# Optimization experiments

Measured on AMD Instinct MI355X. Metric: run time of the kernel, lower is better.

The kernel has to match this reference:

```python
import jax, jax.numpy as jnp
import numpy as np

B, S, D, H, L, V = 8, 512, 1024, 16, 12, 30145
FF = 4 * D
NL = 2  # n_langs
EPS = 1e-12


def _ln(x, g, b):
    m = jnp.mean(x, axis=-1, keepdims=True)
    v = jnp.var(x, axis=-1, keepdims=True)
    return (x - m) * jax.lax.rsqrt(v + EPS) * g + b


def setup_inputs() -> dict:
    key = jax.random.key(0)
    ks = iter(jax.random.split(key, 32))
    std, estd = 0.02, 0.02
    d = {
        "input_ids": jax.random.randint(next(ks), (B, S), 0, V),
        "langs": jax.random.randint(next(ks), (B, S), 0, NL),
        "attention_mask": jnp.ones((B, S), jnp.float32),
        "word_emb": jax.random.normal(next(ks), (V, D), jnp.float32) * estd,
        "pos_emb": jax.random.normal(next(ks), (S, D), jnp.float32) * estd,
        "lang_emb": jax.random.normal(next(ks), (NL, D), jnp.float32) * estd,
        "ln_emb_g": jnp.ones((D,), jnp.float32),
        "ln_emb_b": jnp.zeros((D,), jnp.float32),
        "Wq": jax.random.normal(next(ks), (L, D, D), jnp.float32) * std,
        "bq": jnp.zeros((L, D), jnp.float32),
        "Wk": jax.random.normal(next(ks), (L, D, D), jnp.float32) * std,
        "bk": jnp.zeros((L, D), jnp.float32),
        "Wv": jax.random.normal(next(ks), (L, D, D), jnp.float32) * std,
        "bv": jnp.zeros((L, D), jnp.float32),
        "Wo": jax.random.normal(next(ks), (L, D, D), jnp.float32) * std,
        "bo": jnp.zeros((L, D), jnp.float32),
        "ln1_g": jnp.ones((L, D), jnp.float32),
        "ln1_b": jnp.zeros((L, D), jnp.float32),
        "W1": jax.random.normal(next(ks), (L, D, FF), jnp.float32) * std,
        "b1": jnp.zeros((L, FF), jnp.float32),
        "W2": jax.random.normal(next(ks), (L, FF, D), jnp.float32) * std,
        "b2": jnp.zeros((L, D), jnp.float32),
        "ln2_g": jnp.ones((L, D), jnp.float32),
        "ln2_b": jnp.zeros((L, D), jnp.float32),
    }
    return d


def reference(input_ids, langs, attention_mask, word_emb, pos_emb, lang_emb,
              ln_emb_g, ln_emb_b, Wq, bq, Wk, bk, Wv, bv, Wo, bo,
              ln1_g, ln1_b, W1, b1, W2, b2, ln2_g, ln2_b):
    dh = D // H
    scale = 1.0 / np.sqrt(dh).astype(np.float32)
    # embeddings: word + position + language, then LayerNorm, then pad-mask
    x = word_emb[input_ids] + pos_emb[None, :, :] + lang_emb[langs]  # [B,S,D]
    x = _ln(x, ln_emb_g, ln_emb_b)
    fmask = attention_mask  # [B,S], 1=keep
    x = x * fmask[:, :, None]
    neg = (-1e30) * (1.0 - fmask)[:, None, None, :]  # [B,1,1,S] additive mask

    def layer(x, p):
        Wq_, bq_, Wk_, bk_, Wv_, bv_, Wo_, bo_, g1, gb1, W1_, b1_, W2_, b2_, g2, gb2 = p
        q = ((x @ Wq_ + bq_) * scale).reshape(B, S, H, dh)
        k = (x @ Wk_ + bk_).reshape(B, S, H, dh)
        v = (x @ Wv_ + bv_).reshape(B, S, H, dh)
        scores = jnp.einsum('bqhd,bkhd->bhqk', q, k) + neg
        w = jax.nn.softmax(scores, axis=-1)
        ctx = jnp.einsum('bhqk,bkhd->bqhd', w, v).reshape(B, S, D)
        x = _ln(x + ctx @ Wo_ + bo_, g1, gb1)
        h = jax.nn.gelu(x @ W1_ + b1_, approximate=False)  # erf gelu as in source
        x = _ln(x + h @ W2_ + b2_, g2, gb2)
        x = x * fmask[:, :, None]
        return x, None

    params = (Wq, bq, Wk, bk, Wv, bv, Wo, bo, ln1_g, ln1_b, W1, b1, W2, b2, ln2_g, ln2_b)
    x, _ = jax.lax.scan(layer, x, params)
    return x
```

## Files before the change

### kernel.cpp

```cpp
#include <hip/hip_runtime.h>
#include <math.h>

typedef float  f32x4  __attribute__((ext_vector_type(4)));
typedef __bf16 bf16x8 __attribute__((ext_vector_type(8)));
typedef __bf16 bf16x4 __attribute__((ext_vector_type(4)));

#define DEV __device__ __forceinline__

DEV f32x4 mfma16(bf16x8 a, bf16x8 b, f32x4 c) {
    return __builtin_amdgcn_mfma_f32_16x16x32_bf16(a, b, c, 0, 0, 0);
}

DEV void async16(const void* g, void* l) {
    __builtin_amdgcn_global_load_lds((const __attribute__((address_space(1))) void*)g,
                                     (__attribute__((address_space(3))) void*)l, 16, 0, 0);
}

constexpr int B_  = 8;
constexpr int S_  = 512;
constexpr int D_  = 1024;
constexpr int H_  = 16;
constexpr int FF_ = 4096;
constexpr int ROWS = B_ * S_;

__global__ __launch_bounds__(256)
void embed_ln_kernel(const int* __restrict__ ids, const int* __restrict__ lgs,
                     const float* __restrict__ fmask,
                     const float* __restrict__ wemb, const float* __restrict__ pemb,
                     const float* __restrict__ lemb,
                     const float* __restrict__ g, const float* __restrict__ bb,
                     float* __restrict__ xf, __bf16* __restrict__ xb)
{
    __shared__ float2 red[4];
    const int row = blockIdx.x;
    const int s   = row & (S_ - 1);
    const int t   = threadIdx.x;
    const int lane = t & 63, w = t >> 6;
    const int id = ids[row], lg = lgs[row];

    float4 wv = *(const float4*)(wemb + ((size_t)id << 10) + t * 4);
    float4 pv = *(const float4*)(pemb + ((size_t)s  << 10) + t * 4);
    float4 lv = *(const float4*)(lemb + ((size_t)lg << 10) + t * 4);
    float a[4] = { wv.x + pv.x + lv.x, wv.y + pv.y + lv.y,
                   wv.z + pv.z + lv.z, wv.w + pv.w + lv.w };

    float sm = a[0] + a[1] + a[2] + a[3];
    float sq = a[0]*a[0] + a[1]*a[1] + a[2]*a[2] + a[3]*a[3];
#pragma unroll
    for (int o = 32; o > 0; o >>= 1) { sm += __shfl_down(sm, o); sq += __shfl_down(sq, o); }
    if (lane == 0) red[w] = make_float2(sm, sq);
    __syncthreads();
    float ts = red[0].x + red[1].x + red[2].x + red[3].x;
    float tq = red[0].y + red[1].y + red[2].y + red[3].y;
    float mean = ts * (1.0f / D_);
    float var  = tq * (1.0f / D_) - mean * mean;
    float rs   = rsqrtf(var + 1e-12f);
    float fm   = fmask[row];

    float4 gv = *(const float4*)(g  + t * 4);
    float4 bv = *(const float4*)(bb + t * 4);
    float o0 = ((a[0]-mean)*rs*gv.x + bv.x) * fm;
    float o1 = ((a[1]-mean)*rs*gv.y + bv.y) * fm;
    float o2 = ((a[2]-mean)*rs*gv.z + bv.z) * fm;
    float o3 = ((a[3]-mean)*rs*gv.w + bv.w) * fm;
    *(float4*)(xf + ((size_t)row << 10) + t * 4) = make_float4(o0, o1, o2, o3);
    bf16x4 ob; ob[0] = (__bf16)o0; ob[1] = (__bf16)o1; ob[2] = (__bf16)o2; ob[3] = (__bf16)o3;
    *(bf16x4*)(xb + ((size_t)row << 10) + t * 4) = ob;
}

template<int NP>
__global__ __launch_bounds__(256)
void ln_resN_kernel(const float* __restrict__ xin, const __bf16* __restrict__ yp,
                    const float* __restrict__ g, const float* __restrict__ bb,
                    const float* __restrict__ fmask,
                    float* __restrict__ xf_out, __bf16* __restrict__ xb_out)
{
    constexpr size_t MN = (size_t)ROWS * D_;
    __shared__ float2 red[4];
    const int row = blockIdx.x;
    const int t   = threadIdx.x;
    const int lane = t & 63, w = t >> 6;
    const size_t base = ((size_t)row << 10) + t * 4;

    float4 xv = *(const float4*)(xin + base);
    float a[4] = { xv.x, xv.y, xv.z, xv.w };
#pragma unroll
    for (int pslice = 0; pslice < NP; ++pslice) {
        bf16x4 yv = *(const bf16x4*)(yp + base + (size_t)pslice * MN);
#pragma unroll
        for (int j = 0; j < 4; ++j) a[j] += (float)yv[j];
    }

    float sm = a[0] + a[1] + a[2] + a[3];
    float sq = a[0]*a[0] + a[1]*a[1] + a[2]*a[2] + a[3]*a[3];
#pragma unroll
    for (int o = 32; o > 0; o >>= 1) { sm += __shfl_down(sm, o); sq += __shfl_down(sq, o); }
    if (lane == 0) red[w] = make_float2(sm, sq);
    __syncthreads();
    float ts = red[0].x + red[1].x + red[2].x + red[3].x;
    float tq = red[0].y + red[1].y + red[2].y + red[3].y;
    float mean = ts * (1.0f / D_);
    float var  = tq * (1.0f / D_) - mean * mean;
    float rs   = rsqrtf(var + 1e-12f);
    float fm   = fmask ? fmask[row] : 1.0f;

    float4 gv = *(const float4*)(g  + t * 4);
    float4 bv = *(const float4*)(bb + t * 4);
    float o0 = ((a[0]-mean)*rs*gv.x + bv.x) * fm;
    float o1 = ((a[1]-mean)*rs*gv.y + bv.y) * fm;
    float o2 = ((a[2]-mean)*rs*gv.z + bv.z) * fm;
    float o3 = ((a[3]-mean)*rs*gv.w + bv.w) * fm;
    *(float4*)(xf_out + base) = make_float4(o0, o1, o2, o3);
    bf16x4 ob; ob[0] = (__bf16)o0; ob[1] = (__bf16)o1; ob[2] = (__bf16)o2; ob[3] = (__bf16)o3;
    *(bf16x4*)(xb_out + base) = ob;
}

__global__ __launch_bounds__(256)
void conv_all_kernel(const float* __restrict__ Wq, const float* __restrict__ Wk,
                     const float* __restrict__ Wv, const float* __restrict__ Wo,
                     const float* __restrict__ W1, const float* __restrict__ W2,
                     __bf16* __restrict__ qkvT, __bf16* __restrict__ woT,
                     __bf16* __restrict__ w1T, __bf16* __restrict__ w2T)
{
    __shared__ __bf16 tile[64][66];
    const int id = blockIdx.x;
    const float* src; __bf16* dst; int K, N, t;
    if (id < 1024) {
        const int m = id >> 8; t = id & 255; K = 1024; N = 1024;
        src = (m == 0) ? Wq : (m == 1) ? Wk : (m == 2) ? Wv : Wo;
        dst = (m == 3) ? woT : qkvT + (size_t)m * 1024 * 1024;
    } else if (id < 2048) {
        t = id - 1024; K = 1024; N = 4096; src = W1; dst = w1T;
    } else {
        t = id - 2048; K = 4096; N = 1024; src = W2; dst = w2T;
    }
    const int ktiles = K >> 6;
    const int tk = t % ktiles, tn = t / ktiles;
    const int k0 = tk << 6, n0 = tn << 6;
    const int tt = threadIdx.x;
#pragma unroll
    for (int i = 0; i < 16; ++i) {
        int idx = i * 256 + tt;
        int r = idx >> 6, c = idx & 63;
        tile[c][r] = (__bf16)src[(size_t)(k0 + r) * N + n0 + c];
    }
    __syncthreads();
#pragma unroll
    for (int i = 0; i < 16; ++i) {
        int idx = i * 256 + tt;
        int r = idx >> 6, c = idx & 63;
        dst[(size_t)(n0 + r) * K + k0 + c] = tile[r][c];
    }
}

template<int EPI>
__global__ __launch_bounds__(512, 2)
void gemm256_kernel(const __bf16* __restrict__ A, const __bf16* __restrict__ Bt,
                    const float* __restrict__ b0, const float* __restrict__ b1,
                    const float* __restrict__ b2,
                    __bf16* __restrict__ o0, __bf16* __restrict__ o1,
                    __bf16* __restrict__ o2, __bf16* __restrict__ oP,
                    int M, int N, int K, int Kloc, int nTn, int tiles)
{
    __shared__ __bf16 lds[65536];
    const int tid  = threadIdx.x;
    const int lane = tid & 63;
    const int w    = tid >> 6;
    const int wr   = w >> 2, wc = w & 3;

    const int nwg = gridDim.x, bid = blockIdx.x;
    const int cpx = nwg >> 3;
    const int bswz = (bid & 7) * cpx + (bid >> 3);
    const int slice = bswz / tiles;
    const int tile  = bswz % tiles;
    const int bm = tile / nTn, bn = tile % nTn;
    const int m0 = bm << 8, n0 = bn << 8;
    const int ks = slice * Kloc;

    const int rrT = tid >> 3;
    const size_t swzK  = (size_t)(((tid & 7) ^ (rrT & 7)) * 8);
    const size_t aoff0 = (size_t)rrT * K + swzK;
    const size_t boff0 = (size_t)((rrT >> 5) * 64 + (rrT & 31)) * K + swzK;
    const size_t boff1 = (size_t)(((rrT >> 5) + 2) * 64 + (rrT & 31)) * K + swzK;
    const int wub = w * 512;

    const int aread = (wr * 64 + (lane & 15)) * 64;
    const int bread = (wc * 32 + (lane & 15)) * 64;
    const int csw0 = ((      (lane >> 4) * 16) ^ ((lane & 7) << 4)) >> 1;
    const int csw1 = ((64 +  (lane >> 4) * 16) ^ ((lane & 7) << 4)) >> 1;

    f32x4 acc[8][4] = {};
    bf16x8 a_[4][2], b_[2][2];

#define ST_A(p,h,kt) do {                                                     \
    const size_t gb = (size_t)(m0 + (h) * 64) * K + (kt);                     \
    async16(A + gb + aoff0,                  lds + ((p)*2+(h))*8192 + wub);   \
    async16(A + gb + (size_t)128*K + aoff0,  lds + ((p)*2+(h))*8192 + 4096 + wub); \
} while (0)
#define ST_B(p,h,kt) do {                                                     \
    const size_t gb = (size_t)(n0 + (h) * 32) * K + (kt);                     \
    async16(Bt + gb + boff0, lds + 32768 + ((p)*2+(h))*8192 + wub);           \
    async16(Bt + gb + boff1, lds + 32768 + ((p)*2+(h))*8192 + 4096 + wub);    \
} while (0)
#define DS_A(p,h) do {                                                        \
    const __bf16* base_ = lds + ((p)*2+(h))*8192 + aread;                     \
    _Pragma("unroll") for (int m_ = 0; m_ < 4; ++m_) {                        \
        a_[m_][0] = *(const bf16x8*)(base_ + m_*1024 + csw0);                 \
        a_[m_][1] = *(const bf16x8*)(base_ + m_*1024 + csw1);                 \
    }                                                                         \
} while (0)
#define DS_B(p,h) do {                                                        \
    const __bf16* base_ = lds + 32768 + ((p)*2+(h))*8192 + bread;             \
    _Pragma("unroll") for (int n_ = 0; n_ < 2; ++n_) {                        \
        b_[n_][0] = *(const bf16x8*)(base_ + n_*1024 + csw0);                 \
        b_[n_][1] = *(const bf16x8*)(base_ + n_*1024 + csw1);                 \
    }                                                                         \
} while (0)
#define MM(mb,nb) do {                                                        \
    _Pragma("unroll") for (int m_ = 0; m_ < 4; ++m_)                          \
    _Pragma("unroll") for (int n_ = 0; n_ < 2; ++n_)                          \
    _Pragma("unroll") for (int k_ = 0; k_ < 2; ++k_)                          \
        acc[(mb)+m_][(nb)+n_] = mfma16(a_[m_][k_], b_[n_][k_], acc[(mb)+m_][(nb)+n_]); \
} while (0)
#define SYNC do { __builtin_amdgcn_s_barrier();                               \
    asm volatile("s_waitcnt lgkmcnt(0)" ::: "memory");                        \
    __builtin_amdgcn_s_setprio(1); } while (0)
#define PEND do { __builtin_amdgcn_s_setprio(0);                              \
    __builtin_amdgcn_s_barrier(); } while (0)

    ST_A(0,0, ks);      ST_B(0,1, ks);      ST_A(0,1, ks);      ST_B(0,0, ks);
    ST_A(1,0, ks + 64); ST_B(1,1, ks + 64); ST_A(1,1, ks + 64);
    asm volatile("s_waitcnt vmcnt(6)" ::: "memory");
    __builtin_amdgcn_s_barrier();

    const int nIter = Kloc >> 7;
    for (int i = 0; i < nIter; ++i) {
        const bool nl = (i != nIter - 1);
        const int kt1 = ks + (2*i+1) * 64;
        const int kt2 = ks + (2*i+2) * 64;
        const int kt3 = kt2 + 64;
        DS_A(0,0); DS_B(0,0); ST_B(1,0,kt1);
        SYNC; MM(0,0); PEND;
        DS_B(0,1); if (nl) ST_A(0,0,kt2);
        SYNC; MM(0,2); PEND;
        DS_A(0,1); if (nl) ST_B(0,1,kt2);
        SYNC; MM(4,2); PEND;
        DS_B(0,0); if (nl) ST_A(0,1,kt2);
        SYNC; MM(4,0);
        __builtin_amdgcn_s_setprio(0);
        if (nl) asm volatile("s_waitcnt vmcnt(6)" ::: "memory");
        else    asm volatile("s_waitcnt vmcnt(0)" ::: "memory");
        __builtin_amdgcn_s_barrier();
        DS_A(1,0); DS_B(1,0); if (nl) ST_B(0,0,kt2);
        SYNC; MM(0,0); PEND;
        DS_B(1,1); if (nl) ST_A(1,0,kt3);
        SYNC; MM(0,2); PEND;
        DS_A(1,1); if (nl) ST_B(1,1,kt3);
        SYNC; MM(4,2); PEND;
        DS_B(1,0); if (nl) ST_A(1,1,kt3);
        SYNC; MM(4,0);
        __builtin_amdgcn_s_setprio(0);
        if (nl) asm volatile("s_waitcnt vmcnt(6)" ::: "memory");
        __builtin_amdgcn_s_barrier();
    }
#undef ST_A
#undef ST_B
#undef DS_A
#undef DS_B
#undef MM
#undef SYNC
#undef PEND

    const int mrow = m0 + wr * 128 + (lane >> 4) * 4;
    const int ncol = n0 + wc * 64 + (lane & 15);
    if (EPI == 0) {
        const int sel = n0 >> 10;
        const int nc = ncol & 1023;
        if (sel < 2) {
            __bf16* out = (sel == 0) ? o0 : o1;
            const float* bp = (sel == 0) ? b0 : b1;
            const float scl = (sel == 0) ? 0.125f : 1.0f;
#pragma unroll
            for (int ni = 0; ni < 4; ++ni) {
                const float bvv = bp[nc + ni * 16];
#pragma unroll
                for (int mi = 0; mi < 8; ++mi)
#pragma unroll
                    for (int r = 0; r < 4; ++r)
                        out[(size_t)(mrow + mi * 16 + r) * D_ + nc + ni * 16] =
                            (__bf16)((acc[mi][ni][r] + bvv) * scl);
            }
        } else {
#pragma unroll
            for (int ni = 0; ni < 4; ++ni) {
                const int dhf = nc + ni * 16;
                const float bvv = b2[dhf];
                const int hh = dhf >> 6, dh = dhf & 63;
#pragma unroll
                for (int mi = 0; mi < 8; ++mi) {
                    const int gm0 = mrow + mi * 16;
                    const int bb_ = gm0 >> 9, s0 = gm0 & 511;
                    bf16x4 pk;
#pragma unroll
                    for (int r = 0; r < 4; ++r) pk[r] = (__bf16)(acc[mi][ni][r] + bvv);
                    *(bf16x4*)(o2 + ((size_t)((bb_ * 16 + hh) * 64 + dh) << 9) + s0) = pk;
                }
            }
        }
    } else if (EPI == 2) {
#pragma unroll
        for (int ni = 0; ni < 4; ++ni) {
            const float bvv = b0[ncol + ni * 16];
#pragma unroll
            for (int mi = 0; mi < 8; ++mi)
#pragma unroll
                for (int r = 0; r < 4; ++r) {
                    float v = acc[mi][ni][r] + bvv;
                    float ge = 0.5f * v * (1.0f + erff(v * 0.70710678118654752f));
                    o0[(size_t)(mrow + mi * 16 + r) * N + ncol + ni * 16] = (__bf16)ge;
                }
        }
    } else {
        __bf16* Y = oP + (size_t)slice * M * N;
#pragma unroll
        for (int ni = 0; ni < 4; ++ni) {
            const float bvv = (slice == 0) ? b0[ncol + ni * 16] : 0.0f;
#pragma unroll
            for (int mi = 0; mi < 8; ++mi)
#pragma unroll
                for (int r = 0; r < 4; ++r)
                    Y[(size_t)(mrow + mi * 16 + r) * N + ncol + ni * 16] =
                        (__bf16)(acc[mi][ni][r] + bvv);
        }
    }
}

__global__ __launch_bounds__(256, 2)
void gemm_kernel(const __bf16* __restrict__ A, const __bf16* __restrict__ Bt,
                 const float* __restrict__ bias, __bf16* __restrict__ Cb,
                 int M, int N, int K)
{
    __shared__ __bf16 As[128 * 64];
    __shared__ __bf16 Bs[128 * 64];
    const int tid = threadIdx.x;
    const int lane = tid & 63;
    const int w = tid >> 6, wr = w >> 1, wc = w & 1;
    const int nT = N >> 7;
    const int nwg = gridDim.x;
    const int bid = blockIdx.x;
    const int cpx = nwg >> 3;
    const int bswz = (bid & 7) * cpx + (bid >> 3);
    const int bm = bswz / nT, bn = bswz % nT;
    const int m0 = bm << 7, n0 = bn << 7;

    f32x4 acc[4][4] = {};

    const int chr = tid >> 3, chc = tid & 7;
    const __bf16* ga = A  + (size_t)(m0 + chr) * K + chc * 8;
    const __bf16* gb = Bt + (size_t)(n0 + chr) * K + chc * 8;
    char* la = (char*)As + (tid & ~63) * 16;
    char* lb = (char*)Bs + (tid & ~63) * 16;

    const __bf16* arow = As + (wr * 64 + (lane & 15)) * 64 + (lane >> 4) * 8;
    const __bf16* brow = Bs + (wc * 64 + (lane & 15)) * 64 + (lane >> 4) * 8;

    for (int k0 = 0; k0 < K; k0 += 64) {
#pragma unroll
        for (int i = 0; i < 4; ++i) {
            async16(ga + (size_t)(i * 32) * K + k0, la + i * 4096);
            async16(gb + (size_t)(i * 32) * K + k0, lb + i * 4096);
        }
        __syncthreads();
#pragma unroll
        for (int kk = 0; kk < 2; ++kk) {
            bf16x8 af[4], bf[4];
#pragma unroll
            for (int i = 0; i < 4; ++i) af[i] = *(const bf16x8*)(arow + i * 16 * 64 + kk * 32);
#pragma unroll
            for (int i = 0; i < 4; ++i) bf[i] = *(const bf16x8*)(brow + i * 16 * 64 + kk * 32);
#pragma unroll
            for (int mi = 0; mi < 4; ++mi)
#pragma unroll
                for (int ni = 0; ni < 4; ++ni)
                    acc[mi][ni] = mfma16(af[mi], bf[ni], acc[mi][ni]);
        }
        __syncthreads();
    }

    const int mb = m0 + wr * 64 + ((lane >> 4) * 4);
    const int nb = n0 + wc * 64 + (lane & 15);
#pragma unroll
    for (int ni = 0; ni < 4; ++ni) {
        const float bvv = bias[nb + ni * 16];
#pragma unroll
        for (int mi = 0; mi < 4; ++mi)
#pragma unroll
            for (int r = 0; r < 4; ++r)
                Cb[(size_t)(mb + mi * 16 + r) * N + nb + ni * 16] =
                    (__bf16)(acc[mi][ni][r] + bvv);
    }
}

__global__ __launch_bounds__(256, 2)
void attn_kernel(const __bf16* __restrict__ q, const __bf16* __restrict__ k,
                 const __bf16* __restrict__ vT, const float* __restrict__ fmask,
                 __bf16* __restrict__ ctx)
{
    __shared__ __bf16 Ks[256 * 64];
    __shared__ __bf16 Vt[64 * 256];
    __shared__ float  negm[S_];
    const int bid = blockIdx.x;
    const int qt = bid & 7, h = (bid >> 3) & 15, b = bid >> 7;
    const int tid = threadIdx.x, lane = tid & 63, w = tid >> 6;
    const int g = lane >> 4, q15 = lane & 15, r7 = lane & 7;

    const __bf16* kbase  = k  + ((size_t)b * S_) * D_ + h * 64;
    const __bf16* vTbase = vT + ((size_t)((b * 16 + h) * 64) << 9);
    char* kl = (char*)Ks + (tid & ~63) * 16;
    char* vl = (char*)Vt + (tid & ~63) * 16;
    const int srow  = tid >> 3;
    const int sslot = (tid & 7) ^ (srow & 7);
    const int vrow  = tid >> 5;
#define ST_K(c) do { _Pragma("unroll") for (int i_ = 0; i_ < 8; ++i_) {       \
        const int s_ = (c) * 256 + i_ * 32 + srow;                            \
        async16(kbase + (size_t)s_ * D_ + sslot * 8, kl + i_ * 4096); } } while (0)
#define ST_V(c) do { _Pragma("unroll") for (int i_ = 0; i_ < 8; ++i_) {       \
        const int d_ = i_ * 8 + vrow;                                         \
        async16(vTbase + ((size_t)d_ << 9) + (c) * 256 +                      \
                (((tid & 31) ^ (d_ & 7)) << 3), vl + i_ * 4096); } } while (0)

    ST_K(0);
    for (int i = tid; i < S_; i += 256) negm[i] = (fmask[b * S_ + i] - 1.0f) * 1e30f;

    const __bf16* qbase = q + ((size_t)b * S_ + qt * 64 + w * 16) * D_ + h * 64;
    const bf16x8 qf0 = *(const bf16x8*)(qbase + (size_t)q15 * D_ + g * 8);
    const bf16x8 qf1 = *(const bf16x8*)(qbase + (size_t)q15 * D_ + 32 + g * 8);

    f32x4 sc[32];
#pragma unroll
    for (int i = 0; i < 32; ++i) { sc[i][0] = 0.f; sc[i][1] = 0.f; sc[i][2] = 0.f; sc[i][3] = 0.f; }

#define QKT(c) do { _Pragma("unroll") for (int nf = 0; nf < 16; ++nf) {       \
        const __bf16* kr = Ks + (nf * 16 + q15) * 64;                         \
        const bf16x8 kf0 = *(const bf16x8*)(kr + ((g ^ r7) << 3));            \
        const bf16x8 kf1 = *(const bf16x8*)(kr + (((g + 4) ^ r7) << 3));      \
        sc[(c)*16+nf] = mfma16(kf0, qf0, sc[(c)*16+nf]);                      \
        sc[(c)*16+nf] = mfma16(kf1, qf1, sc[(c)*16+nf]); } } while (0)

    __syncthreads();
    ST_V(0);
    QKT(0);
    __syncthreads();
    ST_K(1);
    __syncthreads();
    QKT(1);

    float mx = -3e38f;
#pragma unroll
    for (int i = 0; i < 32; ++i) {
        const float4 nm4 = *(const float4*)(negm + ((i >> 4) * 256 + (i & 15) * 16 + 4 * g));
        sc[i][0] += nm4.x; sc[i][1] += nm4.y; sc[i][2] += nm4.z; sc[i][3] += nm4.w;
        mx = fmaxf(mx, fmaxf(fmaxf(sc[i][0], sc[i][1]), fmaxf(sc[i][2], sc[i][3])));
    }
    mx = fmaxf(mx, __shfl_xor(mx, 16));
    mx = fmaxf(mx, __shfl_xor(mx, 32));
    float sum = 0.f;
#pragma unroll
    for (int i = 0; i < 32; ++i)
#pragma unroll
        for (int r = 0; r < 4; ++r) { float pp = __expf(sc[i][r] - mx); sc[i][r] = pp; sum += pp; }
    sum += __shfl_xor(sum, 16);
    sum += __shfl_xor(sum, 32);
    const float inv = 1.0f / sum;

    __bf16* P = Ks + w * 4096;
    f32x4 co[4] = {};
#define WR_P(c) do { _Pragma("unroll") for (int i_ = 0; i_ < 16; ++i_) {      \
        bf16x4 pk;                                                            \
        _Pragma("unroll") for (int r = 0; r < 4; ++r) pk[r] = (__bf16)sc[(c)*16+i_][r]; \
        *(bf16x4*)(P + q15 * 256 + ((i_ * 16 + 4 * g) ^ (8 * r7))) = pk; } } while (0)
#define PV() do { _Pragma("unroll") for (int kt = 0; kt < 8; ++kt) {          \
        const bf16x8 pf = *(const bf16x8*)(P + q15 * 256 + ((kt * 32 + 8 * g) ^ (8 * r7))); \
        _Pragma("unroll") for (int nf = 0; nf < 4; ++nf) {                    \
            const int d_ = nf * 16 + q15;                                     \
            const bf16x8 vf = *(const bf16x8*)(Vt + d_ * 256 + ((kt * 32 + 8 * g) ^ (8 * r7))); \
            co[nf] = mfma16(vf, pf, co[nf]); } } } while (0)

    __syncthreads();
    WR_P(0);
    __syncthreads();
    PV();
    __syncthreads();
    WR_P(1);
    ST_V(1);
    __syncthreads();
    PV();
#undef ST_K
#undef ST_V
#undef QKT
#undef WR_P
#undef PV

    __bf16* cb = ctx + ((size_t)b * S_ + qt * 64 + w * 16 + q15) * D_ + h * 64;
#pragma unroll
    for (int nf = 0; nf < 4; ++nf) {
        bf16x4 o4;
#pragma unroll
        for (int r = 0; r < 4; ++r) o4[r] = (__bf16)(co[nf][r] * inv);
        *(bf16x4*)(cb + nf * 16 + 4 * g) = o4;
    }
}

extern "C" void kernel_launch(void* const* d_in, const int* in_sizes, int n_in,
                              void* d_out, int out_size, void* d_ws, size_t ws_size,
                              hipStream_t stream)
{
    (void)in_sizes; (void)n_in; (void)out_size; (void)ws_size;
    const int*   ids   = (const int*)d_in[0];
    const int*   lgs   = (const int*)d_in[1];
    const float* amask = (const float*)d_in[2];
    const float* wemb  = (const float*)d_in[3];
    const float* pemb  = (const float*)d_in[4];
    const float* lemb  = (const float*)d_in[5];
    const float* lng   = (const float*)d_in[6];
    const float* lnbv  = (const float*)d_in[7];
    const float* Wq = (const float*)d_in[8];  const float* bq = (const float*)d_in[9];
    const float* Wk = (const float*)d_in[10]; const float* bk = (const float*)d_in[11];
    const float* Wv = (const float*)d_in[12]; const float* bv = (const float*)d_in[13];
    const float* Wo = (const float*)d_in[14]; const float* bo = (const float*)d_in[15];
    const float* g1 = (const float*)d_in[16]; const float* be1 = (const float*)d_in[17];
    const float* W1 = (const float*)d_in[18]; const float* b1 = (const float*)d_in[19];
    const float* W2 = (const float*)d_in[20]; const float* b2 = (const float*)d_in[21];
    const float* g2 = (const float*)d_in[22]; const float* be2 = (const float*)d_in[23];

    char* p = (char*)d_ws;
    auto take = [&](size_t n) { char* r = p; p += (n + 255) & ~(size_t)255; return r; };
    float*  xf    = (float*) take((size_t)ROWS * D_ * 4);
    __bf16* xb    = (__bf16*)take((size_t)ROWS * D_ * 2);
    __bf16* qb    = (__bf16*)take((size_t)ROWS * D_ * 2);
    __bf16* kb    = (__bf16*)take((size_t)ROWS * D_ * 2);
    __bf16* vT    = (__bf16*)take((size_t)ROWS * D_ * 2);
    __bf16* cxb   = (__bf16*)take((size_t)ROWS * D_ * 2);
    __bf16* hb    = (__bf16*)take((size_t)ROWS * FF_ * 2);
    __bf16* ybp   = (__bf16*)take((size_t)4 * ROWS * D_ * 2);
    __bf16* wqkvT = (__bf16*)take((size_t)3 * D_ * D_ * 2);
    __bf16* woT   = (__bf16*)take((size_t)D_ * D_ * 2);
    __bf16* w1T   = (__bf16*)take((size_t)D_ * FF_ * 2);
    __bf16* w2T   = (__bf16*)take((size_t)FF_ * D_ * 2);

    const int gQKV = (ROWS / 256) * (3 * D_ / 256);
    const int gF1  = (ROWS / 256) * (FF_ / 256);
    const int gF2  = 4 * (ROWS / 256) * (D_ / 256);
    const int gWo  = (ROWS / 128) * (D_ / 128);

    embed_ln_kernel<<<ROWS, 256, 0, stream>>>(ids, lgs, amask, wemb, pemb, lemb, lng, lnbv, xf, xb);

    for (int l = 0; l < 12; ++l) {
        const size_t woff = (size_t)l * D_ * D_;
        const size_t foff = (size_t)l * D_ * FF_;
        conv_all_kernel<<<3072, 256, 0, stream>>>(Wq + woff, Wk + woff, Wv + woff, Wo + woff,
                                                  W1 + foff, W2 + foff,
                                                  wqkvT, woT, w1T, w2T);

        gemm256_kernel<0><<<gQKV, 512, 0, stream>>>(xb, wqkvT, bq + l * D_, bk + l * D_, bv + l * D_,
                                                    qb, kb, vT, nullptr,
                                                    ROWS, 3 * D_, D_, D_, 12, gQKV);

        attn_kernel<<<B_ * H_ * (S_ / 64), 256, 0, stream>>>(qb, kb, vT, amask, cxb);

        gemm_kernel<<<gWo, 256, 0, stream>>>(cxb, woT, bo + l * D_, ybp, ROWS, D_, D_);
        ln_resN_kernel<1><<<ROWS, 256, 0, stream>>>(xf, ybp, g1 + l * D_, be1 + l * D_,
                                                    nullptr, xf, xb);

        gemm256_kernel<2><<<gF1, 512, 0, stream>>>(xb, w1T, b1 + l * FF_, nullptr, nullptr,
                                                   hb, nullptr, nullptr, nullptr,
                                                   ROWS, FF_, D_, D_, 16, gF1);
        gemm256_kernel<3><<<gF2, 512, 0, stream>>>(hb, w2T, b2 + l * D_, nullptr, nullptr,
                                                   nullptr, nullptr, nullptr, ybp,
                                                   ROWS, D_, FF_, D_, 4, 64);

        float* dst = (l == 11) ? (float*)d_out : xf;
        ln_resN_kernel<4><<<ROWS, 256, 0, stream>>>(xf, ybp, g2 + l * D_, be2 + l * D_,
                                                    amask, dst, xb);
    }
}
```

Baseline: 2.592 ms.

## Keep residual in bf16, batch weight conversion, use split-K 256 GEMM for Wo

The fp32 residual stream is replaced by the bf16 copy: the layernorm kernels read and write only bf16 and emit fp32 only for the final output. All 12 layers' weights are converted and transposed to bf16 in one launch before the layer loop, instead of one conversion launch per layer. The Wo projection now runs on the 256-tile GEMM with 4-way split-K, and the dedicated 128-tile GEMM kernel is removed. This cuts residual memory traffic and launch count, but the residual loses precision by staying in bf16 across layers, and the workspace grows to hold every layer's converted weights.

New measurement: 2.587 ms. Within noise of the previous version (-0.2%).

```diff
diff --git a/kernel.cpp b/kernel.cpp
--- a/kernel.cpp
+++ b/kernel.cpp
@@ -29,7 +29,7 @@
                      const float* __restrict__ wemb, const float* __restrict__ pemb,
                      const float* __restrict__ lemb,
                      const float* __restrict__ g, const float* __restrict__ bb,
-                     float* __restrict__ xf, __bf16* __restrict__ xb)
+                     __bf16* __restrict__ xb)
 {
     __shared__ float2 red[4];
     const int row = blockIdx.x;
@@ -59,21 +59,20 @@
 
     float4 gv = *(const float4*)(g  + t * 4);
     float4 bv = *(const float4*)(bb + t * 4);
-    float o0 = ((a[0]-mean)*rs*gv.x + bv.x) * fm;
-    float o1 = ((a[1]-mean)*rs*gv.y + bv.y) * fm;
-    float o2 = ((a[2]-mean)*rs*gv.z + bv.z) * fm;
-    float o3 = ((a[3]-mean)*rs*gv.w + bv.w) * fm;
-    *(float4*)(xf + ((size_t)row << 10) + t * 4) = make_float4(o0, o1, o2, o3);
-    bf16x4 ob; ob[0] = (__bf16)o0; ob[1] = (__bf16)o1; ob[2] = (__bf16)o2; ob[3] = (__bf16)o3;
+    bf16x4 ob;
+    ob[0] = (__bf16)(((a[0]-mean)*rs*gv.x + bv.x) * fm);
+    ob[1] = (__bf16)(((a[1]-mean)*rs*gv.y + bv.y) * fm);
+    ob[2] = (__bf16)(((a[2]-mean)*rs*gv.z + bv.z) * fm);
+    ob[3] = (__bf16)(((a[3]-mean)*rs*gv.w + bv.w) * fm);
     *(bf16x4*)(xb + ((size_t)row << 10) + t * 4) = ob;
 }
 
 template<int NP>
 __global__ __launch_bounds__(256)
-void ln_resN_kernel(const float* __restrict__ xin, const __bf16* __restrict__ yp,
+void ln_resN_kernel(const __bf16* __restrict__ xres, const __bf16* __restrict__ yp,
                     const float* __restrict__ g, const float* __restrict__ bb,
                     const float* __restrict__ fmask,
-                    float* __restrict__ xf_out, __bf16* __restrict__ xb_out)
+                    __bf16* __restrict__ xb_out, float* __restrict__ fout)
 {
     constexpr size_t MN = (size_t)ROWS * D_;
     __shared__ float2 red[4];
@@ -82,8 +81,8 @@
     const int lane = t & 63, w = t >> 6;
     const size_t base = ((size_t)row << 10) + t * 4;
 
-    float4 xv = *(const float4*)(xin + base);
-    float a[4] = { xv.x, xv.y, xv.z, xv.w };
+    bf16x4 xv = *(const bf16x4*)(xres + base);
+    float a[4] = { (float)xv[0], (float)xv[1], (float)xv[2], (float)xv[3] };
 #pragma unroll
     for (int pslice = 0; pslice < NP; ++pslice) {
         bf16x4 yv = *(const bf16x4*)(yp + base + (size_t)pslice * MN);
@@ -110,9 +109,9 @@
     float o1 = ((a[1]-mean)*rs*gv.y + bv.y) * fm;
     float o2 = ((a[2]-mean)*rs*gv.z + bv.z) * fm;
     float o3 = ((a[3]-mean)*rs*gv.w + bv.w) * fm;
-    *(float4*)(xf_out + base) = make_float4(o0, o1, o2, o3);
     bf16x4 ob; ob[0] = (__bf16)o0; ob[1] = (__bf16)o1; ob[2] = (__bf16)o2; ob[3] = (__bf16)o3;
     *(bf16x4*)(xb_out + base) = ob;
+    if (fout) *(float4*)(fout + base) = make_float4(o0, o1, o2, o3);
 }
 
 __global__ __launch_bounds__(256)
@@ -124,15 +123,20 @@
 {
     __shared__ __bf16 tile[64][66];
     const int id = blockIdx.x;
-    const float* src; __bf16* dst; int K, N, t;
-    if (id < 1024) {
-        const int m = id >> 8; t = id & 255; K = 1024; N = 1024;
-        src = (m == 0) ? Wq : (m == 1) ? Wk : (m == 2) ? Wv : Wo;
-        dst = (m == 3) ? woT : qkvT + (size_t)m * 1024 * 1024;
-    } else if (id < 2048) {
-        t = id - 1024; K = 1024; N = 4096; src = W1; dst = w1T;
+    const int l  = id / 3072;
+    int t = id - l * 3072;
+    const size_t woff = (size_t)l * D_ * D_;
+    const size_t foff = (size_t)l * D_ * FF_;
+    const float* src; __bf16* dst; int K, N;
+    if (t < 1024) {
+        const int m = t >> 8; t &= 255; K = 1024; N = 1024;
+        src = ((m == 0) ? Wq : (m == 1) ? Wk : (m == 2) ? Wv : Wo) + woff;
+        dst = (m == 3) ? (woT + woff)
+                       : (qkvT + (size_t)l * 3 * D_ * D_ + (size_t)m * D_ * D_);
+    } else if (t < 2048) {
+        t -= 1024; K = 1024; N = 4096; src = W1 + foff; dst = w1T + foff;
     } else {
-        t = id - 2048; K = 4096; N = 1024; src = W2; dst = w2T;
+        t -= 2048; K = 4096; N = 1024; src = W2 + foff; dst = w2T + foff;
     }
     const int ktiles = K >> 6;
     const int tk = t % ktiles, tn = t / ktiles;
@@ -336,72 +340,6 @@
 }
 
 __global__ __launch_bounds__(256, 2)
-void gemm_kernel(const __bf16* __restrict__ A, const __bf16* __restrict__ Bt,
-                 const float* __restrict__ bias, __bf16* __restrict__ Cb,
-                 int M, int N, int K)
-{
-    __shared__ __bf16 As[128 * 64];
-    __shared__ __bf16 Bs[128 * 64];
-    const int tid = threadIdx.x;
-    const int lane = tid & 63;
-    const int w = tid >> 6, wr = w >> 1, wc = w & 1;
-    const int nT = N >> 7;
-    const int nwg = gridDim.x;
-    const int bid = blockIdx.x;
-    const int cpx = nwg >> 3;
-    const int bswz = (bid & 7) * cpx + (bid >> 3);
-    const int bm = bswz / nT, bn = bswz % nT;
-    const int m0 = bm << 7, n0 = bn << 7;
-
-    f32x4 acc[4][4] = {};
-
-    const int chr = tid >> 3, chc = tid & 7;
-    const __bf16* ga = A  + (size_t)(m0 + chr) * K + chc * 8;
-    const __bf16* gb = Bt + (size_t)(n0 + chr) * K + chc * 8;
-    char* la = (char*)As + (tid & ~63) * 16;
-    char* lb = (char*)Bs + (tid & ~63) * 16;
-
-    const __bf16* arow = As + (wr * 64 + (lane & 15)) * 64 + (lane >> 4) * 8;
-    const __bf16* brow = Bs + (wc * 64 + (lane & 15)) * 64 + (lane >> 4) * 8;
-
-    for (int k0 = 0; k0 < K; k0 += 64) {
-#pragma unroll
-        for (int i = 0; i < 4; ++i) {
-            async16(ga + (size_t)(i * 32) * K + k0, la + i * 4096);
-            async16(gb + (size_t)(i * 32) * K + k0, lb + i * 4096);
-        }
-        __syncthreads();
-#pragma unroll
-        for (int kk = 0; kk < 2; ++kk) {
-            bf16x8 af[4], bf[4];
-#pragma unroll
-            for (int i = 0; i < 4; ++i) af[i] = *(const bf16x8*)(arow + i * 16 * 64 + kk * 32);
-#pragma unroll
-            for (int i = 0; i < 4; ++i) bf[i] = *(const bf16x8*)(brow + i * 16 * 64 + kk * 32);
-#pragma unroll
-            for (int mi = 0; mi < 4; ++mi)
-#pragma unroll
-                for (int ni = 0; ni < 4; ++ni)
-                    acc[mi][ni] = mfma16(af[mi], bf[ni], acc[mi][ni]);
-        }
-        __syncthreads();
-    }
-
-    const int mb = m0 + wr * 64 + ((lane >> 4) * 4);
-    const int nb = n0 + wc * 64 + (lane & 15);
-#pragma unroll
-    for (int ni = 0; ni < 4; ++ni) {
-        const float bvv = bias[nb + ni * 16];
-#pragma unroll
-        for (int mi = 0; mi < 4; ++mi)
-#pragma unroll
-            for (int r = 0; r < 4; ++r)
-                Cb[(size_t)(mb + mi * 16 + r) * N + nb + ni * 16] =
-                    (__bf16)(acc[mi][ni][r] + bvv);
-    }
-}
-
-__global__ __launch_bounds__(256, 2)
 void attn_kernel(const __bf16* __restrict__ q, const __bf16* __restrict__ k,
                  const __bf16* __restrict__ vT, const float* __restrict__ fmask,
                  __bf16* __restrict__ ctx)
@@ -535,7 +473,6 @@
 
     char* p = (char*)d_ws;
     auto take = [&](size_t n) { char* r = p; p += (n + 255) & ~(size_t)255; return r; };
-    float*  xf    = (float*) take((size_t)ROWS * D_ * 4);
     __bf16* xb    = (__bf16*)take((size_t)ROWS * D_ * 2);
     __bf16* qb    = (__bf16*)take((size_t)ROWS * D_ * 2);
     __bf16* kb    = (__bf16*)take((size_t)ROWS * D_ * 2);
@@ -543,44 +480,48 @@
     __bf16* cxb   = (__bf16*)take((size_t)ROWS * D_ * 2);
     __bf16* hb    = (__bf16*)take((size_t)ROWS * FF_ * 2);
     __bf16* ybp   = (__bf16*)take((size_t)4 * ROWS * D_ * 2);
-    __bf16* wqkvT = (__bf16*)take((size_t)3 * D_ * D_ * 2);
-    __bf16* woT   = (__bf16*)take((size_t)D_ * D_ * 2);
-    __bf16* w1T   = (__bf16*)take((size_t)D_ * FF_ * 2);
-    __bf16* w2T   = (__bf16*)take((size_t)FF_ * D_ * 2);
+    __bf16* wqkvT = (__bf16*)take((size_t)12 * 3 * D_ * D_ * 2);
+    __bf16* woT   = (__bf16*)take((size_t)12 * D_ * D_ * 2);
+    __bf16* w1T   = (__bf16*)take((size_t)12 * D_ * FF_ * 2);
+    __bf16* w2T   = (__bf16*)take((size_t)12 * FF_ * D_ * 2);
 
     const int gQKV = (ROWS / 256) * (3 * D_ / 256);
     const int gF1  = (ROWS / 256) * (FF_ / 256);
     const int gF2  = 4 * (ROWS / 256) * (D_ / 256);
-    const int gWo  = (ROWS / 128) * (D_ / 128);
-
-    embed_ln_kernel<<<ROWS, 256, 0, stream>>>(ids, lgs, amask, wemb, pemb, lemb, lng, lnbv, xf, xb);
+    const int gWo  = 4 * (ROWS / 256) * (D_ / 256);
+
+    conv_all_kernel<<<12 * 3072, 256, 0, stream>>>(Wq, Wk, Wv, Wo, W1, W2,
+                                                   wqkvT, woT, w1T, w2T);
+
+    embed_ln_kernel<<<ROWS, 256, 0, stream>>>(ids, lgs, amask, wemb, pemb, lemb, lng, lnbv, xb);
 
     for (int l = 0; l < 12; ++l) {
-        const size_t woff = (size_t)l * D_ * D_;
-        const size_t foff = (size_t)l * D_ * FF_;
-        conv_all_kernel<<<3072, 256, 0, stream>>>(Wq + woff, Wk + woff, Wv + woff, Wo + woff,
-                                                  W1 + foff, W2 + foff,
-                                                  wqkvT, woT, w1T, w2T);
-
-        gemm256_kernel<0><<<gQKV, 512, 0, stream>>>(xb, wqkvT, bq + l * D_, bk + l * D_, bv + l * D_,
+        __bf16* wqkvL = wqkvT + (size_t)l * 3 * D_ * D_;
+        __bf16* woL   = woT   + (size_t)l * D_ * D_;
+        __bf16* w1L   = w1T   + (size_t)l * D_ * FF_;
+        __bf16* w2L   = w2T   + (size_t)l * FF_ * D_;
+
+        gemm256_kernel<0><<<gQKV, 512, 0, stream>>>(xb, wqkvL, bq + l * D_, bk + l * D_, bv + l * D_,
                                                     qb, kb, vT, nullptr,
                                                     ROWS, 3 * D_, D_, D_, 12, gQKV);
 
         attn_kernel<<<B_ * H_ * (S_ / 64), 256, 0, stream>>>(qb, kb, vT, amask, cxb);
 
-        gemm_kernel<<<gWo, 256, 0, stream>>>(cxb, woT, bo + l * D_, ybp, ROWS, D_, D_);
-        ln_resN_kernel<1><<<ROWS, 256, 0, stream>>>(xf, ybp, g1 + l * D_, be1 + l * D_,
-                                                    nullptr, xf, xb);
-
-        gemm256_kernel<2><<<gF1, 512, 0, stream>>>(xb, w1T, b1 + l * FF_, nullptr, nullptr,
+        gemm256_kernel<3><<<gWo, 512, 0, stream>>>(cxb, woL, bo + l * D_, nullptr, nullptr,
+                                                   nullptr, nullptr, nullptr, ybp,
+                                                   ROWS, D_, D_, D_ / 4, 4, 64);
+        ln_resN_kernel<4><<<ROWS, 256, 0, stream>>>(xb, ybp, g1 + l * D_, be1 + l * D_,
+                                                    nullptr, xb, nullptr);
+
+        gemm256_kernel<2><<<gF1, 512, 0, stream>>>(xb, w1L, b1 + l * FF_, nullptr, nullptr,
                                                    hb, nullptr, nullptr, nullptr,
                                                    ROWS, FF_, D_, D_, 16, gF1);
-        gemm256_kernel<3><<<gF2, 512, 0, stream>>>(hb, w2T, b2 + l * D_, nullptr, nullptr,
+        gemm256_kernel<3><<<gF2, 512, 0, stream>>>(hb, w2L, b2 + l * D_, nullptr, nullptr,
                                                    nullptr, nullptr, nullptr, ybp,
                                                    ROWS, D_, FF_, D_, 4, 64);
 
-        float* dst = (l == 11) ? (float*)d_out : xf;
-        ln_resN_kernel<4><<<ROWS, 256, 0, stream>>>(xf, ybp, g2 + l * D_, be2 + l * D_,
-                                                    amask, dst, xb);
-    }
-}
+        float* dst = (l == 11) ? (float*)d_out : nullptr;
+        ln_resN_kernel<4><<<ROWS, 256, 0, stream>>>(xb, ybp, g2 + l * D_, be2 + l * D_,
+                                                    amask, xb, dst);
+    }
+}
```
